# Kernel optimization log

Measured on AMD Instinct MI355X. Metric: run time of the kernel, lower is better.

The kernel has to match this reference:

```python
import jax, jax.numpy as jnp
import numpy as np

N_NODES = 100000


def gcn_conv(x, row, col, W, b, n_nodes):
    # PyG GCNConv: add self-loops, symmetric normalization, linear, scatter-add, bias
    deg = jnp.zeros((n_nodes,), x.dtype).at[col].add(1.0)
    dinv = jnp.where(deg > 0, jax.lax.rsqrt(deg), 0.0)
    norm = dinv[row] * dinv[col]                      # [E+N]
    h = x @ W                                         # [N, out]
    msg = h[row] * norm[:, None]                      # [E+N, out]
    out = jax.ops.segment_sum(msg, col, num_segments=n_nodes)
    return out + b


def setup_inputs() -> dict:
    key = jax.random.key(0)
    ks = jax.random.split(key, 8)
    E = 1600000
    edge_index = jax.random.randint(ks[0], (2, E), 0, N_NODES, dtype=jnp.int64)
    node_features = jax.random.normal(ks[1], (N_NODES, 16), dtype=jnp.float32)
    W1 = jax.random.normal(ks[2], (16, 32), dtype=jnp.float32) * 0.25
    b1 = jnp.zeros((32,), jnp.float32)
    W2 = jax.random.normal(ks[3], (32, 16), dtype=jnp.float32) * 0.18
    b2 = jnp.zeros((16,), jnp.float32)
    fc_W = jax.random.normal(ks[4], (16, 1), dtype=jnp.float32) * 0.25
    fc_b = jnp.zeros((1,), jnp.float32)
    return {"edge_index": edge_index, "node_features": node_features,
            "W1": W1, "b1": b1, "W2": W2, "b2": b2, "fc_W": fc_W, "fc_b": fc_b}


def reference(edge_index, node_features, W1, b1, W2, b2, fc_W, fc_b):
    n = node_features.shape[0]
    loops = jnp.arange(n, dtype=edge_index.dtype)
    row = jnp.concatenate([edge_index[0], loops])     # sources (with self-loops)
    col = jnp.concatenate([edge_index[1], loops])     # targets (with self-loops)
    x = jax.nn.relu(gcn_conv(node_features, row, col, W1, b1, n))
    # F.dropout with training=False is identity (inference)
    x = jax.nn.relu(gcn_conv(x, row, col, W2, b2, n))
    return x @ fc_W + fc_b
```

## Files before the change

kernel.cpp:

```cpp
#include <hip/hip_runtime.h>
#include <hip/hip_fp16.h>


constexpr int NN  = 100000;
constexpr int FIN = 16;
constexpr int FH  = 32;
constexpr int FO  = 16;

constexpr int BK      = 256;
constexpr int NBUCKET = (NN + BK - 1) / BK;
constexpr int CHUNK   = 8192;
constexpr int CAP     = 5376;

static __device__ __forceinline__ int pack2(float a, float b) {
    __half2 t = __float22half2_rn(make_float2(a, b));
    return *reinterpret_cast<int*>(&t);
}
static __device__ __forceinline__ float2 unpack2(int v) {
    __half2 t = *reinterpret_cast<__half2*>(&v);
    return __half22float2(t);
}

__global__ void init_kernel(int* __restrict__ bcursor) {
    int b = blockIdx.x * blockDim.x + threadIdx.x;
    if (b < NBUCKET) bcursor[b] = b * CAP;
}

__global__ __launch_bounds__(256) void bucket_fill_kernel(
        const int* __restrict__ row, const int* __restrict__ col,
        int* __restrict__ bcursor, int* __restrict__ srow, int E) {
    __shared__ int bcnt[NBUCKET];
    __shared__ int bcur[NBUCKET];
    int t = threadIdx.x;
    int e0 = blockIdx.x * CHUNK;
    int m = E - e0; if (m > CHUNK) m = CHUNK;
    for (int b = t; b < NBUCKET; b += 256) bcnt[b] = 0;
    __syncthreads();
    for (int i = t; i < m; i += 256)
        atomicAdd(&bcnt[col[e0 + i] >> 8], 1);
    __syncthreads();
    for (int b = t; b < NBUCKET; b += 256) {
        int v = bcnt[b];
        bcur[b] = v ? atomicAdd(&bcursor[b], v) : 0;
    }
    __syncthreads();
    for (int i = t; i < m; i += 256) {
        int c = col[e0 + i];
        int r = row[e0 + i];
        int p = atomicAdd(&bcur[c >> 8], 1);
        srow[p] = ((c & (BK - 1)) << 17) | r;
    }
}

__global__ __launch_bounds__(256) void bucket_sort_mm1_kernel(
        const int* __restrict__ bcursor, int* __restrict__ srow,
        int* __restrict__ off, int* __restrict__ cnt, float* __restrict__ dinv,
        const float* __restrict__ x, const float* __restrict__ W1,
        __half* __restrict__ g1, int n) {
    __shared__ int ebuf[CAP];
    __shared__ int sorted[CAP];
    __shared__ int cnt2[BK];
    __shared__ int wsum[4];
    __shared__ int wbase[4];
    __shared__ float w1[FIN * FH];
    int t = threadIdx.x;
    for (int i = t; i < FIN * FH; i += 256) w1[i] = W1[i];
    int lo = blockIdx.x << 8;
    int nodes = n - lo; if (nodes > BK) nodes = BK;
    int s0 = blockIdx.x * CAP;
    int m = bcursor[blockIdx.x] - s0;
    if (m > CAP) m = CAP;
    for (int i = t; i < m; i += 256) ebuf[i] = srow[s0 + i];
    cnt2[t] = 0;
    __syncthreads();
    for (int i = t; i < m; i += 256) atomicAdd(&cnt2[ebuf[i] >> 17], 1);
    __syncthreads();
    int v = cnt2[t];
    int s = v;
    #pragma unroll
    for (int d = 1; d < 64; d <<= 1) {
        int u = __shfl_up(s, d, 64);
        if ((t & 63) >= d) s += u;
    }
    if ((t & 63) == 63) wsum[t >> 6] = s;
    __syncthreads();
    if (t < 4) {
        int b = 0;
        for (int k = 0; k < t; k++) b += wsum[k];
        wbase[t] = b;
    }
    __syncthreads();
    int excl = s + wbase[t >> 6] - v;
    cnt2[t] = excl;
    float di = rsqrtf((float)v + 1.0f);
    if (t < nodes) {
        off[lo + t]  = s0 + excl;
        cnt[lo + t]  = v;
        dinv[lo + t] = di;
    }
    __syncthreads();
    for (int i = t; i < m; i += 256) {
        int pv = ebuf[i];
        int p = atomicAdd(&cnt2[pv >> 17], 1);
        sorted[p] = pv & 0x1FFFF;
    }
    __syncthreads();
    for (int i = t; i < m; i += 256) srow[s0 + i] = sorted[i];
    if (t < nodes) {
        int nd = lo + t;
        float xi[FIN];
        const float4* xv = (const float4*)(x + (long long)nd * FIN);
        #pragma unroll
        for (int i = 0; i < FIN / 4; i++) {
            float4 vv = xv[i];
            xi[4*i] = vv.x; xi[4*i+1] = vv.y; xi[4*i+2] = vv.z; xi[4*i+3] = vv.w;
        }
        float h[FH];
        #pragma unroll
        for (int j = 0; j < FH; j++) h[j] = 0.f;
        #pragma unroll
        for (int i = 0; i < FIN; i++) {
            float xs = xi[i];
            #pragma unroll
            for (int j = 0; j < FH; j++) h[j] += xs * w1[i * FH + j];
        }
        int4* gv = (int4*)(g1 + (long long)nd * FH);
        #pragma unroll
        for (int k = 0; k < 4; k++) {
            gv[k] = make_int4(pack2(h[8*k]*di,   h[8*k+1]*di),
                              pack2(h[8*k+2]*di, h[8*k+3]*di),
                              pack2(h[8*k+4]*di, h[8*k+5]*di),
                              pack2(h[8*k+6]*di, h[8*k+7]*di));
        }
    }
}

constexpr int XS = 36;
__global__ __launch_bounds__(256) void gather_mm2_kernel(
        const int* __restrict__ off, const int* __restrict__ cnt,
        const int* __restrict__ srow, const __half* __restrict__ g1,
        const float* __restrict__ dinv, const float* __restrict__ b1,
        const float* __restrict__ W2, __half* __restrict__ g2, int n) {
    __shared__ float xs[64 * XS];
    __shared__ float w[FH * FO];
    __shared__ float bb[FH];
    int t = threadIdx.x;
    for (int i = t; i < FH * FO; i += 256) w[i] = W2[i];
    if (t < FH) bb[t] = b1[t];
    int nl = t >> 2;
    int q = t & 3;
    int node = blockIdx.x * 64 + nl;
    bool live = node < n;
    float acc[8] = {0.f,0.f,0.f,0.f,0.f,0.f,0.f,0.f};
    float di = 0.f;
    if (live) {
        di = dinv[node];
        {
            int4 raw = ((const int4*)(g1 + (long long)node * FH))[q];
            float2 f0 = unpack2(raw.x), f1 = unpack2(raw.y);
            float2 f2 = unpack2(raw.z), f3 = unpack2(raw.w);
            acc[0] = f0.x; acc[1] = f0.y; acc[2] = f1.x; acc[3] = f1.y;
            acc[4] = f2.x; acc[5] = f2.y; acc[6] = f3.x; acc[7] = f3.y;
        }
        int s = off[node];
        int m = cnt[node];
        int i = 0;
        for (; i + 3 < m; i += 4) {
            int r0 = srow[s + i];
            int r1 = srow[s + i + 1];
            int r2 = srow[s + i + 2];
            int r3 = srow[s + i + 3];
            int4 ra = ((const int4*)(g1 + (long long)r0 * FH))[q];
            int4 rb = ((const int4*)(g1 + (long long)r1 * FH))[q];
            int4 rc = ((const int4*)(g1 + (long long)r2 * FH))[q];
            int4 rd = ((const int4*)(g1 + (long long)r3 * FH))[q];
            float2 u;
            u = unpack2(ra.x); acc[0] += u.x; acc[1] += u.y;
            u = unpack2(ra.y); acc[2] += u.x; acc[3] += u.y;
            u = unpack2(ra.z); acc[4] += u.x; acc[5] += u.y;
            u = unpack2(ra.w); acc[6] += u.x; acc[7] += u.y;
            u = unpack2(rb.x); acc[0] += u.x; acc[1] += u.y;
            u = unpack2(rb.y); acc[2] += u.x; acc[3] += u.y;
            u = unpack2(rb.z); acc[4] += u.x; acc[5] += u.y;
            u = unpack2(rb.w); acc[6] += u.x; acc[7] += u.y;
            u = unpack2(rc.x); acc[0] += u.x; acc[1] += u.y;
            u = unpack2(rc.y); acc[2] += u.x; acc[3] += u.y;
            u = unpack2(rc.z); acc[4] += u.x; acc[5] += u.y;
            u = unpack2(rc.w); acc[6] += u.x; acc[7] += u.y;
            u = unpack2(rd.x); acc[0] += u.x; acc[1] += u.y;
            u = unpack2(rd.y); acc[2] += u.x; acc[3] += u.y;
            u = unpack2(rd.z); acc[4] += u.x; acc[5] += u.y;
            u = unpack2(rd.w); acc[6] += u.x; acc[7] += u.y;
        }
        for (; i < m; i++) {
            int r0 = srow[s + i];
            int4 ra = ((const int4*)(g1 + (long long)r0 * FH))[q];
            float2 u;
            u = unpack2(ra.x); acc[0] += u.x; acc[1] += u.y;
            u = unpack2(ra.y); acc[2] += u.x; acc[3] += u.y;
            u = unpack2(ra.z); acc[4] += u.x; acc[5] += u.y;
            u = unpack2(ra.w); acc[6] += u.x; acc[7] += u.y;
        }
    }
    __syncthreads();
    if (live) {
        float* xr = xs + nl * XS + 8 * q;
        #pragma unroll
        for (int j = 0; j < 8; j++) {
            float a = acc[j] * di + bb[8*q + j];
            xr[j] = a > 0.f ? a : 0.f;
        }
    }
    __syncthreads();
    if (live) {
        const float* xr = xs + nl * XS;
        int k0 = 4 * q;
        float o0 = 0.f, o1 = 0.f, o2 = 0.f, o3 = 0.f;
        #pragma unroll
        for (int j = 0; j < FH; j++) {
            float xj = xr[j];
            const float* wr = w + j * FO + k0;
            o0 += xj * wr[0];
            o1 += xj * wr[1];
            o2 += xj * wr[2];
            o3 += xj * wr[3];
        }
        ((int2*)(g2 + (long long)node * FO))[q] =
            make_int2(pack2(o0 * di, o1 * di), pack2(o2 * di, o3 * di));
    }
}

__global__ __launch_bounds__(256) void gather_fc_kernel(
        const int* __restrict__ off, const int* __restrict__ cnt,
        const int* __restrict__ srow, const __half* __restrict__ g2,
        const float* __restrict__ dinv, const float* __restrict__ b2,
        const float* __restrict__ fcW, const float* __restrict__ fcb,
        float* __restrict__ out, int n) {
    __shared__ float w[FO];
    __shared__ float bb[FO];
    __shared__ float fb;
    int t = threadIdx.x;
    if (t < FO) { w[t] = fcW[t]; bb[t] = b2[t]; }
    if (t == 0) fb = fcb[0];
    __syncthreads();
    int node = blockIdx.x * 128 + (t >> 1);
    int q = t & 1;
    if (node >= n) return;
    float di = dinv[node];
    float acc[8];
    {
        int4 raw = ((const int4*)(g2 + (long long)node * FO))[q];
        float2 f0 = unpack2(raw.x), f1 = unpack2(raw.y);
        float2 f2 = unpack2(raw.z), f3 = unpack2(raw.w);
        acc[0] = f0.x; acc[1] = f0.y; acc[2] = f1.x; acc[3] = f1.y;
        acc[4] = f2.x; acc[5] = f2.y; acc[6] = f3.x; acc[7] = f3.y;
    }
    int s = off[node];
    int m = cnt[node];
    int i = 0;
    for (; i + 3 < m; i += 4) {
        int r0 = srow[s + i];
        int r1 = srow[s + i + 1];
        int r2 = srow[s + i + 2];
        int r3 = srow[s + i + 3];
        int4 ra = ((const int4*)(g2 + (long long)r0 * FO))[q];
        int4 rb = ((const int4*)(g2 + (long long)r1 * FO))[q];
        int4 rc = ((const int4*)(g2 + (long long)r2 * FO))[q];
        int4 rd = ((const int4*)(g2 + (long long)r3 * FO))[q];
        float2 u;
        u = unpack2(ra.x); acc[0] += u.x; acc[1] += u.y;
        u = unpack2(ra.y); acc[2] += u.x; acc[3] += u.y;
        u = unpack2(ra.z); acc[4] += u.x; acc[5] += u.y;
        u = unpack2(ra.w); acc[6] += u.x; acc[7] += u.y;
        u = unpack2(rb.x); acc[0] += u.x; acc[1] += u.y;
        u = unpack2(rb.y); acc[2] += u.x; acc[3] += u.y;
        u = unpack2(rb.z); acc[4] += u.x; acc[5] += u.y;
        u = unpack2(rb.w); acc[6] += u.x; acc[7] += u.y;
        u = unpack2(rc.x); acc[0] += u.x; acc[1] += u.y;
        u = unpack2(rc.y); acc[2] += u.x; acc[3] += u.y;
        u = unpack2(rc.z); acc[4] += u.x; acc[5] += u.y;
        u = unpack2(rc.w); acc[6] += u.x; acc[7] += u.y;
        u = unpack2(rd.x); acc[0] += u.x; acc[1] += u.y;
        u = unpack2(rd.y); acc[2] += u.x; acc[3] += u.y;
        u = unpack2(rd.z); acc[4] += u.x; acc[5] += u.y;
        u = unpack2(rd.w); acc[6] += u.x; acc[7] += u.y;
    }
    for (; i < m; i++) {
        int r0 = srow[s + i];
        int4 ra = ((const int4*)(g2 + (long long)r0 * FO))[q];
        float2 u;
        u = unpack2(ra.x); acc[0] += u.x; acc[1] += u.y;
        u = unpack2(ra.y); acc[2] += u.x; acc[3] += u.y;
        u = unpack2(ra.z); acc[4] += u.x; acc[5] += u.y;
        u = unpack2(ra.w); acc[6] += u.x; acc[7] += u.y;
    }
    float p = 0.f;
    #pragma unroll
    for (int j = 0; j < 8; j++) {
        float a = acc[j] * di + bb[8*q + j];
        p += (a > 0.f ? a : 0.f) * w[8*q + j];
    }
    p += __shfl_down(p, 1, 2);
    if (q == 0) out[node] = p + fb;
}

extern "C" void kernel_launch(void* const* d_in, const int* in_sizes, int n_in,
                              void* d_out, int out_size, void* d_ws, size_t ws_size,
                              hipStream_t stream) {
    const int*   edge = (const int*)d_in[0];
    const float* x    = (const float*)d_in[1];
    const float* W1   = (const float*)d_in[2];
    const float* b1   = (const float*)d_in[3];
    const float* W2   = (const float*)d_in[4];
    const float* b2   = (const float*)d_in[5];
    const float* fcW  = (const float*)d_in[6];
    const float* fcb  = (const float*)d_in[7];
    float* out = (float*)d_out;

    const int E = in_sizes[0] / 2;
    const int n = NN;
    const int* row = edge;
    const int* col = edge + E;

    const size_t nA = (size_t)((n + 127) & ~127);
    char* wsb = (char*)d_ws;
    int*   cnt     = (int*)wsb;
    int*   off     = cnt + nA;
    float* dinv    = (float*)(off + nA);
    int*   bcursor = (int*)(dinv + nA);
    int*   srow    = bcursor + 512;
    int*   srowEnd = srow + (size_t)(NBUCKET + 1) * CAP;
    __half* g1     = (__half*)srowEnd;
    __half* g2     = g1 + (size_t)n * FH;

    const int B = 256;
    const int nChunkBlocks = (E + CHUNK - 1) / CHUNK;

    init_kernel<<<2, B, 0, stream>>>(bcursor);
    bucket_fill_kernel<<<nChunkBlocks, B, 0, stream>>>(row, col, bcursor, srow, E);
    bucket_sort_mm1_kernel<<<NBUCKET, B, 0, stream>>>(bcursor, srow, off, cnt, dinv, x, W1, g1, n);
    gather_mm2_kernel<<<(n + 63) / 64, B, 0, stream>>>(off, cnt, srow, g1, dinv, b1, W2, g2, n);
    gather_fc_kernel<<<(n + 127) / 128, B, 0, stream>>>(off, cnt, srow, g2, dinv, b2, fcW, fcb, out, n);
}
```

Baseline: 152.7 us.

## Pad per-node edge lists to multiples of four and vectorize index loads

Each node's sorted source list is padded to a multiple of four, with entries pointing at a zeroed dummy row appended to g1 and g2. This lets the gather loops load four indices with one int4 load and drop the scalar tail loop. The bucket fill and sort kernels move to 512 threads, and the first matmul is split across two threads per node. Padding enlarges the bucket capacity and the srow traffic, and any bucket that exceeds CAP is silently truncated.

```diff
diff --git a/kernel.cpp b/kernel.cpp
--- a/kernel.cpp
+++ b/kernel.cpp
@@ -10,7 +10,7 @@
 constexpr int BK      = 256;
 constexpr int NBUCKET = (NN + BK - 1) / BK;
 constexpr int CHUNK   = 8192;
-constexpr int CAP     = 5376;
+constexpr int CAP     = 5632;
 
 static __device__ __forceinline__ int pack2(float a, float b) {
     __half2 t = __float22half2_rn(make_float2(a, b));
@@ -21,12 +21,15 @@
     return __half22float2(t);
 }
 
-__global__ void init_kernel(int* __restrict__ bcursor) {
+__global__ void init_kernel(int* __restrict__ bcursor,
+                            __half* __restrict__ g1, __half* __restrict__ g2) {
     int b = blockIdx.x * blockDim.x + threadIdx.x;
     if (b < NBUCKET) bcursor[b] = b * CAP;
-}
-
-__global__ __launch_bounds__(256) void bucket_fill_kernel(
+    if (b < 4) ((int4*)(g1 + (long long)NN * FH))[b] = make_int4(0, 0, 0, 0);
+    else if (b < 6) ((int4*)(g2 + (long long)NN * FO))[b - 4] = make_int4(0, 0, 0, 0);
+}
+
+__global__ __launch_bounds__(512) void bucket_fill_kernel(
         const int* __restrict__ row, const int* __restrict__ col,
         int* __restrict__ bcursor, int* __restrict__ srow, int E) {
     __shared__ int bcnt[NBUCKET];
@@ -34,17 +37,17 @@
     int t = threadIdx.x;
     int e0 = blockIdx.x * CHUNK;
     int m = E - e0; if (m > CHUNK) m = CHUNK;
-    for (int b = t; b < NBUCKET; b += 256) bcnt[b] = 0;
-    __syncthreads();
-    for (int i = t; i < m; i += 256)
+    for (int b = t; b < NBUCKET; b += 512) bcnt[b] = 0;
+    __syncthreads();
+    for (int i = t; i < m; i += 512)
         atomicAdd(&bcnt[col[e0 + i] >> 8], 1);
     __syncthreads();
-    for (int b = t; b < NBUCKET; b += 256) {
+    for (int b = t; b < NBUCKET; b += 512) {
         int v = bcnt[b];
         bcur[b] = v ? atomicAdd(&bcursor[b], v) : 0;
     }
     __syncthreads();
-    for (int i = t; i < m; i += 256) {
+    for (int i = t; i < m; i += 512) {
         int c = col[e0 + i];
         int r = row[e0 + i];
         int p = atomicAdd(&bcur[c >> 8], 1);
@@ -52,7 +55,7 @@
     }
 }
 
-__global__ __launch_bounds__(256) void bucket_sort_mm1_kernel(
+__global__ __launch_bounds__(512) void bucket_sort_mm1_kernel(
         const int* __restrict__ bcursor, int* __restrict__ srow,
         int* __restrict__ off, int* __restrict__ cnt, float* __restrict__ dinv,
         const float* __restrict__ x, const float* __restrict__ W1,
@@ -60,29 +63,36 @@
     __shared__ int ebuf[CAP];
     __shared__ int sorted[CAP];
     __shared__ int cnt2[BK];
+    __shared__ float sdi[BK];
     __shared__ int wsum[4];
     __shared__ int wbase[4];
+    __shared__ int Mtot;
     __shared__ float w1[FIN * FH];
     int t = threadIdx.x;
-    for (int i = t; i < FIN * FH; i += 256) w1[i] = W1[i];
+    for (int i = t; i < FIN * FH; i += 512) w1[i] = W1[i];
     int lo = blockIdx.x << 8;
     int nodes = n - lo; if (nodes > BK) nodes = BK;
     int s0 = blockIdx.x * CAP;
     int m = bcursor[blockIdx.x] - s0;
     if (m > CAP) m = CAP;
-    for (int i = t; i < m; i += 256) ebuf[i] = srow[s0 + i];
-    cnt2[t] = 0;
-    __syncthreads();
-    for (int i = t; i < m; i += 256) atomicAdd(&cnt2[ebuf[i] >> 17], 1);
-    __syncthreads();
-    int v = cnt2[t];
-    int s = v;
-    #pragma unroll
-    for (int d = 1; d < 64; d <<= 1) {
-        int u = __shfl_up(s, d, 64);
-        if ((t & 63) >= d) s += u;
-    }
-    if ((t & 63) == 63) wsum[t >> 6] = s;
+    if (m < 0)  m = 0;
+    for (int i = t; i < m; i += 512) ebuf[i] = srow[s0 + i];
+    if (t < BK) cnt2[t] = 0;
+    __syncthreads();
+    for (int i = t; i < m; i += 512) atomicAdd(&cnt2[ebuf[i] >> 17], 1);
+    __syncthreads();
+    int v = 0, pv = 0, s = 0, excl = 0;
+    if (t < BK) {
+        v  = cnt2[t];
+        pv = (v + 3) & ~3;
+        s  = pv;
+        #pragma unroll
+        for (int d = 1; d < 64; d <<= 1) {
+            int u = __shfl_up(s, d, 64);
+            if ((t & 63) >= d) s += u;
+        }
+        if ((t & 63) == 63) wsum[t >> 6] = s;
+    }
     __syncthreads();
     if (t < 4) {
         int b = 0;
@@ -90,24 +100,36 @@
         wbase[t] = b;
     }
     __syncthreads();
-    int excl = s + wbase[t >> 6] - v;
-    cnt2[t] = excl;
-    float di = rsqrtf((float)v + 1.0f);
-    if (t < nodes) {
-        off[lo + t]  = s0 + excl;
-        cnt[lo + t]  = v;
-        dinv[lo + t] = di;
-    }
-    __syncthreads();
-    for (int i = t; i < m; i += 256) {
-        int pv = ebuf[i];
-        int p = atomicAdd(&cnt2[pv >> 17], 1);
-        sorted[p] = pv & 0x1FFFF;
-    }
-    __syncthreads();
-    for (int i = t; i < m; i += 256) srow[s0 + i] = sorted[i];
-    if (t < nodes) {
-        int nd = lo + t;
+    if (t < BK) {
+        excl = s + wbase[t >> 6] - pv;
+        cnt2[t] = excl;
+        float di = rsqrtf((float)v + 1.0f);
+        sdi[t] = di;
+        if (t < nodes) {
+            off[lo + t]  = s0 + excl;
+            cnt[lo + t]  = v;
+            dinv[lo + t] = di;
+        }
+        if (t == BK - 1) Mtot = excl + pv;
+    }
+    __syncthreads();
+    for (int i = t; i < m; i += 512) {
+        int pvv = ebuf[i];
+        int p = atomicAdd(&cnt2[pvv >> 17], 1);
+        sorted[p] = pvv & 0x1FFFF;
+    }
+    __syncthreads();
+    if (t < BK) {
+        for (int p = excl + v; p < excl + pv; p++) sorted[p] = NN;
+    }
+    __syncthreads();
+    int M = Mtot; if (M > CAP) M = CAP;
+    for (int i = t; i < M; i += 512) srow[s0 + i] = sorted[i];
+    int lane = t >> 8;
+    int nd0  = t & 255;
+    if (nd0 < nodes) {
+        int nd = lo + nd0;
+        float di = sdi[nd0];
         float xi[FIN];
         const float4* xv = (const float4*)(x + (long long)nd * FIN);
         #pragma unroll
@@ -115,23 +137,21 @@
             float4 vv = xv[i];
             xi[4*i] = vv.x; xi[4*i+1] = vv.y; xi[4*i+2] = vv.z; xi[4*i+3] = vv.w;
         }
-        float h[FH];
-        #pragma unroll
-        for (int j = 0; j < FH; j++) h[j] = 0.f;
+        float h[16];
+        #pragma unroll
+        for (int j = 0; j < 16; j++) h[j] = 0.f;
+        const float* wl = w1 + lane * 16;
         #pragma unroll
         for (int i = 0; i < FIN; i++) {
             float xs = xi[i];
             #pragma unroll
-            for (int j = 0; j < FH; j++) h[j] += xs * w1[i * FH + j];
-        }
-        int4* gv = (int4*)(g1 + (long long)nd * FH);
-        #pragma unroll
-        for (int k = 0; k < 4; k++) {
-            gv[k] = make_int4(pack2(h[8*k]*di,   h[8*k+1]*di),
-                              pack2(h[8*k+2]*di, h[8*k+3]*di),
-                              pack2(h[8*k+4]*di, h[8*k+5]*di),
-                              pack2(h[8*k+6]*di, h[8*k+7]*di));
-        }
+            for (int j = 0; j < 16; j++) h[j] += xs * wl[i * FH + j];
+        }
+        int4* gv = (int4*)(g1 + (long long)nd * FH) + lane * 2;
+        gv[0] = make_int4(pack2(h[0]*di,  h[1]*di),  pack2(h[2]*di,  h[3]*di),
+                          pack2(h[4]*di,  h[5]*di),  pack2(h[6]*di,  h[7]*di));
+        gv[1] = make_int4(pack2(h[8]*di,  h[9]*di),  pack2(h[10]*di, h[11]*di),
+                          pack2(h[12]*di, h[13]*di), pack2(h[14]*di, h[15]*di));
     }
 }
 
@@ -164,16 +184,12 @@
         }
         int s = off[node];
         int m = cnt[node];
-        int i = 0;
-        for (; i + 3 < m; i += 4) {
-            int r0 = srow[s + i];
-            int r1 = srow[s + i + 1];
-            int r2 = srow[s + i + 2];
-            int r3 = srow[s + i + 3];
-            int4 ra = ((const int4*)(g1 + (long long)r0 * FH))[q];
-            int4 rb = ((const int4*)(g1 + (long long)r1 * FH))[q];
-            int4 rc = ((const int4*)(g1 + (long long)r2 * FH))[q];
-            int4 rd = ((const int4*)(g1 + (long long)r3 * FH))[q];
+        for (int i = 0; i < m; i += 4) {
+            int4 ix = *(const int4*)(srow + s + i);
+            int4 ra = ((const int4*)(g1 + (long long)ix.x * FH))[q];
+            int4 rb = ((const int4*)(g1 + (long long)ix.y * FH))[q];
+            int4 rc = ((const int4*)(g1 + (long long)ix.z * FH))[q];
+            int4 rd = ((const int4*)(g1 + (long long)ix.w * FH))[q];
             float2 u;
             u = unpack2(ra.x); acc[0] += u.x; acc[1] += u.y;
             u = unpack2(ra.y); acc[2] += u.x; acc[3] += u.y;
@@ -192,15 +208,6 @@
             u = unpack2(rd.z); acc[4] += u.x; acc[5] += u.y;
             u = unpack2(rd.w); acc[6] += u.x; acc[7] += u.y;
         }
-        for (; i < m; i++) {
-            int r0 = srow[s + i];
-            int4 ra = ((const int4*)(g1 + (long long)r0 * FH))[q];
-            float2 u;
-            u = unpack2(ra.x); acc[0] += u.x; acc[1] += u.y;
-            u = unpack2(ra.y); acc[2] += u.x; acc[3] += u.y;
-            u = unpack2(ra.z); acc[4] += u.x; acc[5] += u.y;
-            u = unpack2(ra.w); acc[6] += u.x; acc[7] += u.y;
-        }
     }
     __syncthreads();
     if (live) {
@@ -257,16 +264,12 @@
     }
     int s = off[node];
     int m = cnt[node];
-    int i = 0;
-    for (; i + 3 < m; i += 4) {
-        int r0 = srow[s + i];
-        int r1 = srow[s + i + 1];
-        int r2 = srow[s + i + 2];
-        int r3 = srow[s + i + 3];
-        int4 ra = ((const int4*)(g2 + (long long)r0 * FO))[q];
-        int4 rb = ((const int4*)(g2 + (long long)r1 * FO))[q];
-        int4 rc = ((const int4*)(g2 + (long long)r2 * FO))[q];
-        int4 rd = ((const int4*)(g2 + (long long)r3 * FO))[q];
+    for (int i = 0; i < m; i += 4) {
+        int4 ix = *(const int4*)(srow + s + i);
+        int4 ra = ((const int4*)(g2 + (long long)ix.x * FO))[q];
+        int4 rb = ((const int4*)(g2 + (long long)ix.y * FO))[q];
+        int4 rc = ((const int4*)(g2 + (long long)ix.z * FO))[q];
+        int4 rd = ((const int4*)(g2 + (long long)ix.w * FO))[q];
         float2 u;
         u = unpack2(ra.x); acc[0] += u.x; acc[1] += u.y;
         u = unpack2(ra.y); acc[2] += u.x; acc[3] += u.y;
@@ -285,15 +288,6 @@
         u = unpack2(rd.z); acc[4] += u.x; acc[5] += u.y;
         u = unpack2(rd.w); acc[6] += u.x; acc[7] += u.y;
     }
-    for (; i < m; i++) {
-        int r0 = srow[s + i];
-        int4 ra = ((const int4*)(g2 + (long long)r0 * FO))[q];
-        float2 u;
-        u = unpack2(ra.x); acc[0] += u.x; acc[1] += u.y;
-        u = unpack2(ra.y); acc[2] += u.x; acc[3] += u.y;
-        u = unpack2(ra.z); acc[4] += u.x; acc[5] += u.y;
-        u = unpack2(ra.w); acc[6] += u.x; acc[7] += u.y;
-    }
     float p = 0.f;
     #pragma unroll
     for (int j = 0; j < 8; j++) {
@@ -331,14 +325,13 @@
     int*   srow    = bcursor + 512;
     int*   srowEnd = srow + (size_t)(NBUCKET + 1) * CAP;
     __half* g1     = (__half*)srowEnd;
-    __half* g2     = g1 + (size_t)n * FH;
-
-    const int B = 256;
+    __half* g2     = g1 + (size_t)(n + 1) * FH;
+
     const int nChunkBlocks = (E + CHUNK - 1) / CHUNK;
 
-    init_kernel<<<2, B, 0, stream>>>(bcursor);
-    bucket_fill_kernel<<<nChunkBlocks, B, 0, stream>>>(row, col, bcursor, srow, E);
-    bucket_sort_mm1_kernel<<<NBUCKET, B, 0, stream>>>(bcursor, srow, off, cnt, dinv, x, W1, g1, n);
-    gather_mm2_kernel<<<(n + 63) / 64, B, 0, stream>>>(off, cnt, srow, g1, dinv, b1, W2, g2, n);
-    gather_fc_kernel<<<(n + 127) / 128, B, 0, stream>>>(off, cnt, srow, g2, dinv, b2, fcW, fcb, out, n);
-}
+    init_kernel<<<2, 256, 0, stream>>>(bcursor, g1, g2);
+    bucket_fill_kernel<<<nChunkBlocks, 512, 0, stream>>>(row, col, bcursor, srow, E);
+    bucket_sort_mm1_kernel<<<NBUCKET, 512, 0, stream>>>(bcursor, srow, off, cnt, dinv, x, W1, g1, n);
+    gather_mm2_kernel<<<(n + 63) / 64, 256, 0, stream>>>(off, cnt, srow, g1, dinv, b1, W2, g2, n);
+    gather_fc_kernel<<<(n + 127) / 128, 256, 0, stream>>>(off, cnt, srow, g2, dinv, b2, fcW, fcb, out, n);
+}
```

Measured after the change: 145.5 us. -4.7%, faster.
